# Optimization experiments

Hardware: AMD Instinct MI355X
Metric: run time of the kernel (lower is better)

The kernel has to match this reference:

```python
import jax, jax.numpy as jnp
import numpy as np

B, N = 4, 1024
D_MODEL, N_HEADS, D_HEAD, D_COORD = 512, 8, 64, 2


def setup_inputs() -> dict:
    key = jax.random.key(0)
    ks = jax.random.split(key, 8)
    sd = 1.0 / np.sqrt(D_MODEL)
    return {
        "x": jax.random.normal(ks[0], (B, N, D_MODEL), dtype=jnp.float32),
        "positions": jax.random.uniform(ks[1], (N, D_COORD), dtype=jnp.float32) * 32.0,
        "W_Q": jax.random.normal(ks[2], (D_MODEL, N_HEADS * D_HEAD), dtype=jnp.float32) * sd,
        "W_K": jax.random.normal(ks[3], (D_MODEL, N_HEADS * D_HEAD), dtype=jnp.float32) * sd,
        "W_V": jax.random.normal(ks[4], (D_MODEL, N_HEADS * D_HEAD), dtype=jnp.float32) * sd,
        "W_O": jax.random.normal(ks[5], (N_HEADS * D_HEAD, D_MODEL), dtype=jnp.float32) * sd,
        "U": jax.random.normal(ks[6], (N_HEADS, D_HEAD, D_HEAD), dtype=jnp.float32),
        "freqs": jax.random.normal(ks[7], (N_HEADS, D_HEAD // 2, D_COORD), dtype=jnp.float32),
    }


def reference(x, positions, W_Q, W_K, W_V, W_O, U, freqs):
    # x: (B,N,d_model); positions: (N,d_coord); U: (H,dh,dh); freqs: (H,m,d_coord)
    Bn, Nn, _ = x.shape
    H, dh, _ = U.shape
    m = dh // 2
    scale = (dh // 2) ** -0.5

    Q = (x @ W_Q).reshape(Bn, Nn, H, dh)
    K = (x @ W_K).reshape(Bn, Nn, H, dh)
    V = (x @ W_V).reshape(Bn, Nn, H, dh)

    # Active-subspace projector: Pi = qr(U)[0] @ qr(U)[0].T per head
    Uq = jax.vmap(lambda u: jnp.linalg.qr(u)[0])(U)              # (H,dh,dh)
    P = jnp.einsum('hde,hfe->hdf', Uq, Uq)                       # U U^T
    Qp = jnp.einsum('bnhd,hdf->bhnf', Q, P)                      # (B,H,N,dh)
    Kp = jnp.einsum('bnhd,hdf->bhnf', K, P)

    # Relative rotation: R_rel(r_j - r_i) is block-diag 2x2 rotations with
    # angle theta_ijm = freqs_m . (r_j - r_i) = a_jm - a_im (separable), so
    # q^T R(r_j-r_i) k = (R(a_i)q)^T (R(a_j)k)  -- exact RoPE identity.
    ang = jnp.einsum('nc,hmc->hnm', positions, freqs)            # (H,N,m)
    c = jnp.cos(ang)[None]                                       # (1,H,N,m)
    s = jnp.sin(ang)[None]

    def rot(v):  # v: (B,H,N,dh) -> rotated (even, odd) halves (B,H,N,m)
        ve, vo = v[..., ::2], v[..., 1::2]
        return ve * c - vo * s, ve * s + vo * c

    qe, qo = rot(Qp)
    ke, ko = rot(Kp)
    scores = (jnp.einsum('bhim,bhjm->bhij', qe, ke)
              + jnp.einsum('bhim,bhjm->bhij', qo, ko)) * scale   # (B,H,N,N)
    w = jax.nn.softmax(scores, axis=-1)
    out = jnp.einsum('bhij,bjhd->bihd', w, V).reshape(Bn, Nn, H * dh)
    return out @ W_O
```

## Files before the change

### kernel.cpp

```cpp
#include <hip/hip_runtime.h>
#include <math.h>

#define NBATCH 4
#define NSEQ   1024
#define DMODEL 512
#define NH     8
#define DH     64
#define MROWS  (NBATCH*NSEQ)
#define MHALF  (DH/2)

typedef __attribute__((ext_vector_type(8))) short bf16x8;
typedef __attribute__((ext_vector_type(4))) float floatx4;

__device__ __forceinline__ ushort f2bf(float f) {
    union { float f; uint u; } v; v.f = f;
    uint r = v.u + 0x7fffu + ((v.u >> 16) & 1u);
    return (ushort)(r >> 16);
}

__global__ __launch_bounds__(256) void prep_kernel(
    const float* __restrict__ pos, const float* __restrict__ freqs,
    const float* __restrict__ x,
    const float* __restrict__ Wq, const float* __restrict__ Wk,
    const float* __restrict__ Wv, const float* __restrict__ Wo,
    float* __restrict__ cosT, float* __restrict__ sinT,
    ushort* __restrict__ xb, ushort* __restrict__ Wt)
{
    __shared__ float T[64][65];
    const int bid = blockIdx.x;
    const int tid = threadIdx.x;

    if (bid < 1024) {
        int idx = bid * 256 + tid;
        int m = idx & 31;
        int n = (idx >> 5) & 1023;
        int h = idx >> 15;
        float a = pos[n*2+0] * freqs[(h*MHALF+m)*2+0]
                + pos[n*2+1] * freqs[(h*MHALF+m)*2+1];
        cosT[idx] = cosf(a);
        sinT[idx] = sinf(a);
    } else if (bid < 2048) {
        int idx = ((bid - 1024) * 256 + tid) * 8;
        float4 a = *(const float4*)&x[idx];
        float4 b = *(const float4*)&x[idx+4];
        uint4 pk;
        pk.x = (uint)f2bf(a.x) | ((uint)f2bf(a.y) << 16);
        pk.y = (uint)f2bf(a.z) | ((uint)f2bf(a.w) << 16);
        pk.z = (uint)f2bf(b.x) | ((uint)f2bf(b.y) << 16);
        pk.w = (uint)f2bf(b.z) | ((uint)f2bf(b.w) << 16);
        *(uint4*)&xb[idx] = pk;
    } else {
        int b2 = bid - 2048;
        int n0g = (b2 & 31) * 64;
        int k0  = (b2 >> 5) * 64;
        int mat = n0g >> 9;
        const float* W = (mat == 0) ? Wq : ((mat == 1) ? Wk : ((mat == 2) ? Wv : Wo));
        int n0 = n0g & 511;
        int c = tid & 63, r = tid >> 6;
        #pragma unroll
        for (int i = 0; i < 16; i++)
            T[r + i*4][c] = W[(k0 + r + i*4) * DMODEL + n0 + c];
        __syncthreads();
        int nl = tid >> 2;
        int kg = tid & 3;
        #pragma unroll
        for (int g = 0; g < 4; g++) {
            int kl = kg * 16 + g * 4;
            uint2 pk;
            pk.x = (uint)f2bf(T[kl+0][nl]) | ((uint)f2bf(T[kl+1][nl]) << 16);
            pk.y = (uint)f2bf(T[kl+2][nl]) | ((uint)f2bf(T[kl+3][nl]) << 16);
            *(uint2*)&Wt[(size_t)(n0g + nl) * DMODEL + k0 + kl] = pk;
        }
    }
}

__global__ __launch_bounds__(256) void qkv_gemm(
    const ushort* __restrict__ xb, const ushort* __restrict__ Wt,
    const float* __restrict__ cosT, const float* __restrict__ sinT,
    ushort* __restrict__ Qb, ushort* __restrict__ Kb, ushort* __restrict__ Vt)
{
    __shared__ ushort As[64 * 40];
    __shared__ ushort Bs[64 * 40];
    __shared__ float  Cs[64][65];

    const int cb = blockIdx.x;
    const int rb = blockIdx.y;
    const int mat = cb >> 3;
    const int c0 = (cb & 7) * 64;
    const int r0 = rb * 64;
    const int ng0 = mat * 512 + c0;

    const int tid = threadIdx.x;
    const int w = tid >> 6, l = tid & 63;
    const int lr = l & 15, lg = l >> 4;

    const int srow = tid >> 2;
    const int sgrp = tid & 3;

    floatx4 acc[4];
    #pragma unroll
    for (int nt = 0; nt < 4; nt++) acc[nt] = (floatx4){0.f,0.f,0.f,0.f};

    for (int k0 = 0; k0 < DMODEL; k0 += 32) {
        __syncthreads();
        *(uint4*)&As[srow*40 + sgrp*8] =
            *(const uint4*)&xb[(size_t)(r0 + srow) * DMODEL + k0 + sgrp*8];
        *(uint4*)&Bs[srow*40 + sgrp*8] =
            *(const uint4*)&Wt[(size_t)(ng0 + srow) * DMODEL + k0 + sgrp*8];
        __syncthreads();

        bf16x8 af = *(const bf16x8*)&As[(16*w + lr)*40 + lg*8];
        #pragma unroll
        for (int nt = 0; nt < 4; nt++) {
            bf16x8 bf = *(const bf16x8*)&Bs[(nt*16 + lr)*40 + lg*8];
            acc[nt] = __builtin_amdgcn_mfma_f32_16x16x32_bf16(af, bf, acc[nt], 0, 0, 0);
        }
    }

    __syncthreads();
    #pragma unroll
    for (int nt = 0; nt < 4; nt++)
        #pragma unroll
        for (int r = 0; r < 4; r++)
            Cs[16*w + lg*4 + r][nt*16 + lr] = acc[nt][r];
    __syncthreads();

    const int tx = tid & 15, ty = tid >> 4;
    const int dbase = tx * 4;
    const int head = c0 >> 6;

    if (mat == 2) {
        int rowbase = r0 + ty * 4;
        int b = rowbase >> 10, n0 = rowbase & 1023;
        size_t vbase = (size_t)(b * NH + head) * DH;
        #pragma unroll
        for (int j = 0; j < 4; j++) {
            ushort us[4];
            #pragma unroll
            for (int i = 0; i < 4; i++) us[i] = f2bf(Cs[ty*4 + i][tx*4 + j]);
            uint2 pk;
            pk.x = (uint)us[0] | ((uint)us[1] << 16);
            pk.y = (uint)us[2] | ((uint)us[3] << 16);
            *(uint2*)&Vt[(vbase + dbase + j) * NSEQ + n0] = pk;
        }
    } else {
        ushort* dst = (mat == 0) ? Qb : Kb;
        #pragma unroll
        for (int i = 0; i < 4; i++) {
            int row = r0 + ty * 4 + i;
            int b = row >> 10, n = row & 1023;
            float v[4];
            #pragma unroll
            for (int p = 0; p < 2; p++) {
                int de = dbase + 2 * p;
                int m = de >> 1;
                float c = cosT[(head * NSEQ + n) * MHALF + m];
                float s = sinT[(head * NSEQ + n) * MHALF + m];
                float ve = Cs[ty*4 + i][tx*4 + 2*p];
                float vo = Cs[ty*4 + i][tx*4 + 2*p + 1];
                v[2*p]     = ve * c - vo * s;
                v[2*p + 1] = ve * s + vo * c;
            }
            uint2 pk;
            pk.x = (uint)f2bf(v[0]) | ((uint)f2bf(v[1]) << 16);
            pk.y = (uint)f2bf(v[2]) | ((uint)f2bf(v[3]) << 16);
            *(uint2*)&dst[((size_t)(b * NH + head) * NSEQ + n) * DH + dbase] = pk;
        }
    }
}

__global__ __launch_bounds__(256, 4) void attn_kernel(
    const ushort* __restrict__ Qb, const ushort* __restrict__ Kb,
    const ushort* __restrict__ Vt, float* __restrict__ Opart,
    float* __restrict__ Lsum)
{
    __shared__ ushort Ks[64 * 72];
    __shared__ ushort Vs[64 * 72];
    __shared__ ushort Ps[128 * 72];

    const int tid = threadIdx.x;
    const int w = tid >> 6, l = tid & 63;
    const int lr = l & 15, lg = l >> 4;
    const int bh = blockIdx.y, q0 = blockIdx.x * 128;
    const int z = blockIdx.z, jt0 = z * 4;

    const ushort* Qg = Qb + (size_t)bh * NSEQ * DH;
    const ushort* Kg = Kb + (size_t)bh * NSEQ * DH;
    const ushort* Vg = Vt + (size_t)bh * DH * NSEQ;

    bf16x8 qf[2][2];
    #pragma unroll
    for (int qc = 0; qc < 2; qc++)
        #pragma unroll
        for (int ks = 0; ks < 2; ks++)
            qf[qc][ks] = *(const bf16x8*)(Qg +
                (size_t)(q0 + 32*w + 16*qc + lr) * DH + ks*32 + lg*8);

    floatx4 ot[4][2];
    #pragma unroll
    for (int dt = 0; dt < 4; dt++)
        #pragma unroll
        for (int qc = 0; qc < 2; qc++)
            ot[dt][qc] = (floatx4){0.f, 0.f, 0.f, 0.f};
    float rsum[2] = {0.f, 0.f};
    const float cexp = 0.2550348550f;

    const int sr = tid >> 2;
    const int sc = (tid & 3) * 16;

    const ushort* kp = Kg + (size_t)(jt0*64 + sr) * DH + sc;
    uint4 ka  = *(const uint4*)kp;
    uint4 kb2 = *(const uint4*)(kp + 8);
    const ushort* vp = Vg + (size_t)sr * NSEQ + jt0*64 + sc;
    uint4 va  = *(const uint4*)vp;
    uint4 vb2 = *(const uint4*)(vp + 8);

    for (int jt = jt0; jt < jt0 + 4; jt++) {
        __syncthreads();
        *(uint4*)&Ks[sr*72 + sc]     = ka;
        *(uint4*)&Ks[sr*72 + sc + 8] = kb2;
        *(uint4*)&Vs[sr*72 + sc]     = va;
        *(uint4*)&Vs[sr*72 + sc + 8] = vb2;
        __syncthreads();

        if (jt < jt0 + 3) {
            const ushort* kn = Kg + (size_t)((jt+1)*64 + sr) * DH + sc;
            ka  = *(const uint4*)kn;
            kb2 = *(const uint4*)(kn + 8);
            const ushort* vn = Vg + (size_t)sr * NSEQ + (jt+1)*64 + sc;
            va  = *(const uint4*)vn;
            vb2 = *(const uint4*)(vn + 8);
        }

        #pragma unroll
        for (int jm = 0; jm < 4; jm++) {
            bf16x8 a0 = *(const bf16x8*)&Ks[(jm*16 + lr)*72 + lg*8];
            bf16x8 a1 = *(const bf16x8*)&Ks[(jm*16 + lr)*72 + 32 + lg*8];
            #pragma unroll
            for (int qc = 0; qc < 2; qc++) {
                floatx4 s = (floatx4){0.f, 0.f, 0.f, 0.f};
                s = __builtin_amdgcn_mfma_f32_16x16x32_bf16(a0, qf[qc][0], s, 0, 0, 0);
                s = __builtin_amdgcn_mfma_f32_16x16x32_bf16(a1, qf[qc][1], s, 0, 0, 0);
                ushort us[4];
                #pragma unroll
                for (int r = 0; r < 4; r++) {
                    float p = exp2f(s[r] * cexp);
                    rsum[qc] += p;
                    us[r] = f2bf(p);
                }
                uint2 pk;
                pk.x = (uint)us[0] | ((uint)us[1] << 16);
                pk.y = (uint)us[2] | ((uint)us[3] << 16);
                *(uint2*)&Ps[(32*w + 16*qc + lr)*72 + jm*16 + lg*4] = pk;
            }
        }

        bf16x8 pf[2][2];
        #pragma unroll
        for (int qc = 0; qc < 2; qc++)
            #pragma unroll
            for (int ks = 0; ks < 2; ks++)
                pf[qc][ks] = *(const bf16x8*)&Ps[(32*w + 16*qc + lr)*72 + ks*32 + lg*8];
        #pragma unroll
        for (int dt = 0; dt < 4; dt++) {
            bf16x8 v0 = *(const bf16x8*)&Vs[(dt*16 + lr)*72 + lg*8];
            bf16x8 v1 = *(const bf16x8*)&Vs[(dt*16 + lr)*72 + 32 + lg*8];
            #pragma unroll
            for (int qc = 0; qc < 2; qc++) {
                ot[dt][qc] = __builtin_amdgcn_mfma_f32_16x16x32_bf16(v0, pf[qc][0], ot[dt][qc], 0, 0, 0);
                ot[dt][qc] = __builtin_amdgcn_mfma_f32_16x16x32_bf16(v1, pf[qc][1], ot[dt][qc], 0, 0, 0);
            }
        }
    }

    #pragma unroll
    for (int qc = 0; qc < 2; qc++) {
        rsum[qc] += __shfl_xor(rsum[qc], 16, 64);
        rsum[qc] += __shfl_xor(rsum[qc], 32, 64);
    }

    #pragma unroll
    for (int qc = 0; qc < 2; qc++) {
        int n = q0 + 32*w + 16*qc + lr;
        size_t obase = ((size_t)(z * 32 + bh) * NSEQ + n) * DH;
        #pragma unroll
        for (int dt = 0; dt < 4; dt++)
            *(floatx4*)&Opart[obase + dt*16 + lg*4] = ot[dt][qc];
        if (lg == 0)
            Lsum[(size_t)(z * 32 + bh) * NSEQ + n] = rsum[qc];
    }
}

__global__ __launch_bounds__(256) void combine_kernel(
    const float* __restrict__ Op, const float* __restrict__ Ls,
    ushort* __restrict__ Obb)
{
    int idx = blockIdx.x * 256 + threadIdx.x;
    int qi = idx >> 2;
    int dp = (idx & 3) << 4;
    float inv = 1.f / (Ls[qi] + Ls[32768 + qi] + Ls[65536 + qi] + Ls[98304 + qi]);
    const float* p0 = Op + (size_t)qi * 64 + dp;
    const size_t zs = (size_t)32768 * 64;
    ushort* po = Obb + (size_t)qi * 64 + dp;
    #pragma unroll
    for (int g = 0; g < 4; g++) {
        float4 u0 = *(const float4*)(p0 + g*4);
        float4 u1 = *(const float4*)(p0 + zs + g*4);
        float4 u2 = *(const float4*)(p0 + 2*zs + g*4);
        float4 u3 = *(const float4*)(p0 + 3*zs + g*4);
        float sx = (u0.x + u1.x + u2.x + u3.x) * inv;
        float sy = (u0.y + u1.y + u2.y + u3.y) * inv;
        float sz = (u0.z + u1.z + u2.z + u3.z) * inv;
        float sw = (u0.w + u1.w + u2.w + u3.w) * inv;
        uint2 pk;
        pk.x = (uint)f2bf(sx) | ((uint)f2bf(sy) << 16);
        pk.y = (uint)f2bf(sz) | ((uint)f2bf(sw) << 16);
        *(uint2*)(po + g*4) = pk;
    }
}

__global__ __launch_bounds__(256) void out_gemm(
    const ushort* __restrict__ Obb, const ushort* __restrict__ Wt,
    float* __restrict__ out)
{
    __shared__ ushort As[64 * 40];
    __shared__ ushort Bs[64 * 40];
    __shared__ float  Cs[64][65];

    const int cb = blockIdx.x;
    const int rb = blockIdx.y;
    const int c0 = cb * 64, r0 = rb * 64;

    const int tid = threadIdx.x;
    const int w = tid >> 6, l = tid & 63;
    const int lr = l & 15, lg = l >> 4;
    const int srow = tid >> 2;
    const int sgrp = tid & 3;

    const int arow = r0 + srow;
    const int b = arow >> 10, n = arow & 1023;

    floatx4 acc[4];
    #pragma unroll
    for (int nt = 0; nt < 4; nt++) acc[nt] = (floatx4){0.f,0.f,0.f,0.f};

    for (int k0 = 0; k0 < DMODEL; k0 += 32) {
        int h = k0 >> 6;
        int d0 = k0 & 63;
        __syncthreads();
        *(uint4*)&As[srow*40 + sgrp*8] =
            *(const uint4*)&Obb[((size_t)(b * NH + h) * NSEQ + n) * DH + d0 + sgrp*8];
        *(uint4*)&Bs[srow*40 + sgrp*8] =
            *(const uint4*)&Wt[(size_t)(1536 + c0 + srow) * DMODEL + k0 + sgrp*8];
        __syncthreads();

        bf16x8 af = *(const bf16x8*)&As[(16*w + lr)*40 + lg*8];
        #pragma unroll
        for (int nt = 0; nt < 4; nt++) {
            bf16x8 bf = *(const bf16x8*)&Bs[(nt*16 + lr)*40 + lg*8];
            acc[nt] = __builtin_amdgcn_mfma_f32_16x16x32_bf16(af, bf, acc[nt], 0, 0, 0);
        }
    }

    __syncthreads();
    #pragma unroll
    for (int nt = 0; nt < 4; nt++)
        #pragma unroll
        for (int r = 0; r < 4; r++)
            Cs[16*w + lg*4 + r][nt*16 + lr] = acc[nt][r];
    __syncthreads();

    const int tx = tid & 15, ty = tid >> 4;
    #pragma unroll
    for (int i = 0; i < 4; i++) {
        float4 o;
        o.x = Cs[ty*4 + i][tx*4 + 0];
        o.y = Cs[ty*4 + i][tx*4 + 1];
        o.z = Cs[ty*4 + i][tx*4 + 2];
        o.w = Cs[ty*4 + i][tx*4 + 3];
        *(float4*)&out[(size_t)(r0 + ty*4 + i) * DMODEL + c0 + tx*4] = o;
    }
}

extern "C" void kernel_launch(void* const* d_in, const int* in_sizes, int n_in,
                              void* d_out, int out_size, void* d_ws, size_t ws_size,
                              hipStream_t stream) {
    const float* x         = (const float*)d_in[0];
    const float* positions = (const float*)d_in[1];
    const float* Wq        = (const float*)d_in[2];
    const float* Wk        = (const float*)d_in[3];
    const float* Wv        = (const float*)d_in[4];
    const float* Wo        = (const float*)d_in[5];
    const float* freqs     = (const float*)d_in[7];
    float* out = (float*)d_out;

    float*  ws    = (float*)d_ws;
    float*  cosT  = ws;
    float*  sinT  = cosT + NH*NSEQ*MHALF;
    float*  Opart = sinT + NH*NSEQ*MHALF;
    float*  Lsum  = Opart + 4*(size_t)NBATCH*NH*NSEQ*DH;
    ushort* xb    = (ushort*)(Lsum + 4*(size_t)NBATCH*NH*NSEQ);
    ushort* Wt    = xb + (size_t)MROWS*DMODEL;
    ushort* Qb    = Wt + (size_t)2048*DMODEL;
    ushort* Kb    = Qb + (size_t)NBATCH*NH*NSEQ*DH;
    ushort* Vt    = Kb + (size_t)NBATCH*NH*NSEQ*DH;
    ushort* Obb   = Vt + (size_t)NBATCH*NH*NSEQ*DH;

    prep_kernel<<<dim3(2304), 256, 0, stream>>>(positions, freqs, x, Wq, Wk, Wv, Wo,
                                                cosT, sinT, xb, Wt);
    qkv_gemm<<<dim3(24, 64), 256, 0, stream>>>(xb, Wt, cosT, sinT, Qb, Kb, Vt);
    attn_kernel<<<dim3(8, 32, 4), 256, 0, stream>>>(Qb, Kb, Vt, Opart, Lsum);
    combine_kernel<<<dim3(512), 256, 0, stream>>>(Opart, Lsum, Obb);
    out_gemm<<<dim3(8, 64), 256, 0, stream>>>(Obb, Wt, out);
}
```

Before: 135.3 us.

## Use 128x128 tiles with direct global-to-LDS loads in QKV and output GEMMs

After: 160.4 us. 18.6% more time.

```diff
diff --git a/kernel.cpp b/kernel.cpp
--- a/kernel.cpp
+++ b/kernel.cpp
@@ -16,6 +16,13 @@
     union { float f; uint u; } v; v.f = f;
     uint r = v.u + 0x7fffu + ((v.u >> 16) & 1u);
     return (ushort)(r >> 16);
+}
+
+__device__ __forceinline__ void g2l16(const ushort* g, ushort* l) {
+    __builtin_amdgcn_global_load_lds(
+        (const __attribute__((address_space(1))) uint*)g,
+        (__attribute__((address_space(3))) uint*)l,
+        16, 0, 0);
 }
 
 __global__ __launch_bounds__(256) void prep_kernel(
@@ -79,92 +86,108 @@
     const float* __restrict__ cosT, const float* __restrict__ sinT,
     ushort* __restrict__ Qb, ushort* __restrict__ Kb, ushort* __restrict__ Vt)
 {
-    __shared__ ushort As[64 * 40];
-    __shared__ ushort Bs[64 * 40];
-    __shared__ float  Cs[64][65];
+    __shared__ union {
+        struct { ushort A[128*32]; ushort B[128*32]; } st;
+        float Cs[128*65];
+    } sm;
 
     const int cb = blockIdx.x;
     const int rb = blockIdx.y;
-    const int mat = cb >> 3;
-    const int c0 = (cb & 7) * 64;
-    const int r0 = rb * 64;
-    const int ng0 = mat * 512 + c0;
+    const int r0 = rb * 128;
+    const int ngBase = cb * 128;
+    const int mat = cb >> 2;
 
     const int tid = threadIdx.x;
     const int w = tid >> 6, l = tid & 63;
     const int lr = l & 15, lg = l >> 4;
-
-    const int srow = tid >> 2;
-    const int sgrp = tid & 3;
-
-    floatx4 acc[4];
-    #pragma unroll
-    for (int nt = 0; nt < 4; nt++) acc[nt] = (floatx4){0.f,0.f,0.f,0.f};
+    const int wr = w >> 1, wc = w & 1;
+
+    const int srow  = 32*w + (l >> 2);
+    const int skoff = (l & 3) * 8;
+
+    floatx4 acc[4][4];
+    #pragma unroll
+    for (int mt = 0; mt < 4; mt++)
+        #pragma unroll
+        for (int nt = 0; nt < 4; nt++)
+            acc[mt][nt] = (floatx4){0.f, 0.f, 0.f, 0.f};
 
     for (int k0 = 0; k0 < DMODEL; k0 += 32) {
         __syncthreads();
-        *(uint4*)&As[srow*40 + sgrp*8] =
-            *(const uint4*)&xb[(size_t)(r0 + srow) * DMODEL + k0 + sgrp*8];
-        *(uint4*)&Bs[srow*40 + sgrp*8] =
-            *(const uint4*)&Wt[(size_t)(ng0 + srow) * DMODEL + k0 + sgrp*8];
-        __syncthreads();
-
-        bf16x8 af = *(const bf16x8*)&As[(16*w + lr)*40 + lg*8];
-        #pragma unroll
-        for (int nt = 0; nt < 4; nt++) {
-            bf16x8 bf = *(const bf16x8*)&Bs[(nt*16 + lr)*40 + lg*8];
-            acc[nt] = __builtin_amdgcn_mfma_f32_16x16x32_bf16(af, bf, acc[nt], 0, 0, 0);
-        }
-    }
-
-    __syncthreads();
-    #pragma unroll
-    for (int nt = 0; nt < 4; nt++)
-        #pragma unroll
-        for (int r = 0; r < 4; r++)
-            Cs[16*w + lg*4 + r][nt*16 + lr] = acc[nt][r];
-    __syncthreads();
-
-    const int tx = tid & 15, ty = tid >> 4;
-    const int dbase = tx * 4;
-    const int head = c0 >> 6;
-
-    if (mat == 2) {
-        int rowbase = r0 + ty * 4;
-        int b = rowbase >> 10, n0 = rowbase & 1023;
-        size_t vbase = (size_t)(b * NH + head) * DH;
-        #pragma unroll
-        for (int j = 0; j < 4; j++) {
-            ushort us[4];
-            #pragma unroll
-            for (int i = 0; i < 4; i++) us[i] = f2bf(Cs[ty*4 + i][tx*4 + j]);
-            uint2 pk;
-            pk.x = (uint)us[0] | ((uint)us[1] << 16);
-            pk.y = (uint)us[2] | ((uint)us[3] << 16);
-            *(uint2*)&Vt[(vbase + dbase + j) * NSEQ + n0] = pk;
-        }
-    } else {
-        ushort* dst = (mat == 0) ? Qb : Kb;
-        #pragma unroll
-        for (int i = 0; i < 4; i++) {
-            int row = r0 + ty * 4 + i;
-            int b = row >> 10, n = row & 1023;
-            float v[4];
-            #pragma unroll
-            for (int p = 0; p < 2; p++) {
-                int de = dbase + 2 * p;
-                int m = de >> 1;
-                float c = cosT[(head * NSEQ + n) * MHALF + m];
-                float s = sinT[(head * NSEQ + n) * MHALF + m];
-                float ve = Cs[ty*4 + i][tx*4 + 2*p];
-                float vo = Cs[ty*4 + i][tx*4 + 2*p + 1];
-                v[2*p]     = ve * c - vo * s;
-                v[2*p + 1] = ve * s + vo * c;
+        g2l16(&xb[(size_t)(r0 + srow) * DMODEL + k0 + skoff],          &sm.st.A[(32*w) * 32]);
+        g2l16(&xb[(size_t)(r0 + srow + 16) * DMODEL + k0 + skoff],     &sm.st.A[(32*w + 16) * 32]);
+        g2l16(&Wt[(size_t)(ngBase + srow) * DMODEL + k0 + skoff],      &sm.st.B[(32*w) * 32]);
+        g2l16(&Wt[(size_t)(ngBase + srow + 16) * DMODEL + k0 + skoff], &sm.st.B[(32*w + 16) * 32]);
+        __syncthreads();
+
+        bf16x8 af[4], bf[4];
+        #pragma unroll
+        for (int mt = 0; mt < 4; mt++)
+            af[mt] = *(const bf16x8*)&sm.st.A[(64*wr + mt*16 + lr)*32 + lg*8];
+        #pragma unroll
+        for (int nt = 0; nt < 4; nt++)
+            bf[nt] = *(const bf16x8*)&sm.st.B[(64*wc + nt*16 + lr)*32 + lg*8];
+        #pragma unroll
+        for (int mt = 0; mt < 4; mt++)
+            #pragma unroll
+            for (int nt = 0; nt < 4; nt++)
+                acc[mt][nt] = __builtin_amdgcn_mfma_f32_16x16x32_bf16(af[mt], bf[nt], acc[mt][nt], 0, 0, 0);
+    }
+
+    #pragma unroll
+    for (int ch = 0; ch < 2; ch++) {
+        const int head = (2*cb + ch) & 7;
+        __syncthreads();
+        if (wc == ch) {
+            #pragma unroll
+            for (int mt = 0; mt < 4; mt++)
+                #pragma unroll
+                for (int nt = 0; nt < 4; nt++)
+                    #pragma unroll
+                    for (int r = 0; r < 4; r++)
+                        sm.Cs[(64*wr + mt*16 + lg*4 + r)*65 + nt*16 + lr] = acc[mt][nt][r];
+        }
+        __syncthreads();
+
+        if (mat == 2) {
+            int vn = tid & 31, vd = tid >> 5;
+            int n0v = (r0 & 1023) + vn*4;
+            int bv = r0 >> 10;
+            size_t vbase = (size_t)(bv*8 + head) * 64;
+            #pragma unroll
+            for (int dj = 0; dj < 8; dj++) {
+                int d = vd*8 + dj;
+                ushort us[4];
+                #pragma unroll
+                for (int i = 0; i < 4; i++) us[i] = f2bf(sm.Cs[(vn*4 + i)*65 + d]);
+                uint2 pk;
+                pk.x = (uint)us[0] | ((uint)us[1] << 16);
+                pk.y = (uint)us[2] | ((uint)us[3] << 16);
+                *(uint2*)&Vt[(vbase + d)*NSEQ + n0v] = pk;
             }
-            uint2 pk;
-            pk.x = (uint)f2bf(v[0]) | ((uint)f2bf(v[1]) << 16);
-            pk.y = (uint)f2bf(v[2]) | ((uint)f2bf(v[3]) << 16);
-            *(uint2*)&dst[((size_t)(b * NH + head) * NSEQ + n) * DH + dbase] = pk;
+        } else {
+            ushort* dst = (mat == 0) ? Qb : Kb;
+            int row = tid >> 1;
+            int half = tid & 1;
+            int grow = r0 + row;
+            int bq = grow >> 10, n = grow & 1023;
+            const float* cs  = &sm.Cs[row*65 + half*32];
+            const float* ct  = &cosT[((size_t)head*NSEQ + n)*MHALF + half*16];
+            const float* stt = &sinT[((size_t)head*NSEQ + n)*MHALF + half*16];
+            size_t ob = ((size_t)(bq*NH + head)*NSEQ + n)*DH + half*32;
+            #pragma unroll
+            for (int g = 0; g < 8; g++) {
+                float e0 = cs[g*4+0], o0 = cs[g*4+1];
+                float e1 = cs[g*4+2], o1 = cs[g*4+3];
+                float c0 = ct[g*2],   s0 = stt[g*2];
+                float c1 = ct[g*2+1], s1 = stt[g*2+1];
+                float v0 = e0*c0 - o0*s0, v1 = e0*s0 + o0*c0;
+                float v2 = e1*c1 - o1*s1, v3 = e1*s1 + o1*c1;
+                uint2 pk;
+                pk.x = (uint)f2bf(v0) | ((uint)f2bf(v1) << 16);
+                pk.y = (uint)f2bf(v2) | ((uint)f2bf(v3) << 16);
+                *(uint2*)&dst[ob + g*4] = pk;
+            }
         }
     }
 }
@@ -323,63 +346,65 @@
     const ushort* __restrict__ Obb, const ushort* __restrict__ Wt,
     float* __restrict__ out)
 {
-    __shared__ ushort As[64 * 40];
-    __shared__ ushort Bs[64 * 40];
-    __shared__ float  Cs[64][65];
+    __shared__ struct { ushort A[128*32]; ushort B[128*32]; } sm;
 
     const int cb = blockIdx.x;
     const int rb = blockIdx.y;
-    const int c0 = cb * 64, r0 = rb * 64;
+    const int r0 = rb * 128;
+    const int c0 = cb * 128;
+    const int ngBase = 1536 + c0;
 
     const int tid = threadIdx.x;
     const int w = tid >> 6, l = tid & 63;
     const int lr = l & 15, lg = l >> 4;
-    const int srow = tid >> 2;
-    const int sgrp = tid & 3;
-
-    const int arow = r0 + srow;
-    const int b = arow >> 10, n = arow & 1023;
-
-    floatx4 acc[4];
-    #pragma unroll
-    for (int nt = 0; nt < 4; nt++) acc[nt] = (floatx4){0.f,0.f,0.f,0.f};
+    const int wr = w >> 1, wc = w & 1;
+
+    const int srow  = 32*w + (l >> 2);
+    const int skoff = (l & 3) * 8;
+
+    const int b0 = r0 >> 10;
+    const int nsBase = (r0 & 1023) + srow;
+
+    floatx4 acc[4][4];
+    #pragma unroll
+    for (int mt = 0; mt < 4; mt++)
+        #pragma unroll
+        for (int nt = 0; nt < 4; nt++)
+            acc[mt][nt] = (floatx4){0.f, 0.f, 0.f, 0.f};
 
     for (int k0 = 0; k0 < DMODEL; k0 += 32) {
-        int h = k0 >> 6;
-        int d0 = k0 & 63;
-        __syncthreads();
-        *(uint4*)&As[srow*40 + sgrp*8] =
-            *(const uint4*)&Obb[((size_t)(b * NH + h) * NSEQ + n) * DH + d0 + sgrp*8];
-        *(uint4*)&Bs[srow*40 + sgrp*8] =
-            *(const uint4*)&Wt[(size_t)(1536 + c0 + srow) * DMODEL + k0 + sgrp*8];
-        __syncthreads();
-
-        bf16x8 af = *(const bf16x8*)&As[(16*w + lr)*40 + lg*8];
-        #pragma unroll
-        for (int nt = 0; nt < 4; nt++) {
-            bf16x8 bf = *(const bf16x8*)&Bs[(nt*16 + lr)*40 + lg*8];
-            acc[nt] = __builtin_amdgcn_mfma_f32_16x16x32_bf16(af, bf, acc[nt], 0, 0, 0);
-        }
-    }
-
-    __syncthreads();
-    #pragma unroll
-    for (int nt = 0; nt < 4; nt++)
-        #pragma unroll
-        for (int r = 0; r < 4; r++)
-            Cs[16*w + lg*4 + r][nt*16 + lr] = acc[nt][r];
-    __syncthreads();
-
-    const int tx = tid & 15, ty = tid >> 4;
-    #pragma unroll
-    for (int i = 0; i < 4; i++) {
-        float4 o;
-        o.x = Cs[ty*4 + i][tx*4 + 0];
-        o.y = Cs[ty*4 + i][tx*4 + 1];
-        o.z = Cs[ty*4 + i][tx*4 + 2];
-        o.w = Cs[ty*4 + i][tx*4 + 3];
-        *(float4*)&out[(size_t)(r0 + ty*4 + i) * DMODEL + c0 + tx*4] = o;
-    }
+        const int h = k0 >> 6;
+        const int d0 = (k0 & 63) + skoff;
+        const size_t abase = (size_t)(b0*NH + h) * NSEQ;
+        __syncthreads();
+        g2l16(&Obb[(abase + nsBase) * DH + d0],        &sm.A[(32*w) * 32]);
+        g2l16(&Obb[(abase + nsBase + 16) * DH + d0],   &sm.A[(32*w + 16) * 32]);
+        g2l16(&Wt[(size_t)(ngBase + srow) * DMODEL + k0 + skoff],      &sm.B[(32*w) * 32]);
+        g2l16(&Wt[(size_t)(ngBase + srow + 16) * DMODEL + k0 + skoff], &sm.B[(32*w + 16) * 32]);
+        __syncthreads();
+
+        bf16x8 af[4], bf[4];
+        #pragma unroll
+        for (int mt = 0; mt < 4; mt++)
+            af[mt] = *(const bf16x8*)&sm.A[(64*wr + mt*16 + lr)*32 + lg*8];
+        #pragma unroll
+        for (int nt = 0; nt < 4; nt++)
+            bf[nt] = *(const bf16x8*)&sm.B[(64*wc + nt*16 + lr)*32 + lg*8];
+        #pragma unroll
+        for (int mt = 0; mt < 4; mt++)
+            #pragma unroll
+            for (int nt = 0; nt < 4; nt++)
+                acc[mt][nt] = __builtin_amdgcn_mfma_f32_16x16x32_bf16(af[mt], bf[nt], acc[mt][nt], 0, 0, 0);
+    }
+
+    #pragma unroll
+    for (int mt = 0; mt < 4; mt++)
+        #pragma unroll
+        for (int nt = 0; nt < 4; nt++)
+            #pragma unroll
+            for (int r = 0; r < 4; r++)
+                out[(size_t)(r0 + 64*wr + mt*16 + lg*4 + r) * DMODEL
+                    + c0 + 64*wc + nt*16 + lr] = acc[mt][nt][r];
 }
 
 extern "C" void kernel_launch(void* const* d_in, const int* in_sizes, int n_in,
@@ -408,8 +433,8 @@
 
     prep_kernel<<<dim3(2304), 256, 0, stream>>>(positions, freqs, x, Wq, Wk, Wv, Wo,
                                                 cosT, sinT, xb, Wt);
-    qkv_gemm<<<dim3(24, 64), 256, 0, stream>>>(xb, Wt, cosT, sinT, Qb, Kb, Vt);
+    qkv_gemm<<<dim3(12, 32), 256, 0, stream>>>(xb, Wt, cosT, sinT, Qb, Kb, Vt);
     attn_kernel<<<dim3(8, 32, 4), 256, 0, stream>>>(Qb, Kb, Vt, Opart, Lsum);
     combine_kernel<<<dim3(512), 256, 0, stream>>>(Opart, Lsum, Obb);
-    out_gemm<<<dim3(8, 64), 256, 0, stream>>>(Obb, Wt, out);
-}
+    out_gemm<<<dim3(4, 32), 256, 0, stream>>>(Obb, Wt, out);
+}
```
